# Optimization experiments

Measured on AMD Instinct MI355X. Metric: run time of the kernel, lower is better.

The kernel has to match this reference:

```python
import jax, jax.numpy as jnp
import numpy as np
from jax import lax

EPS = 1e-08


def setup_inputs() -> dict:
    key = jax.random.key(0)
    kX, kY, kXs, kW, kA, kB1, kB2 = jax.random.split(key, 7)
    P, D, K, M = 8192, 1024, 131072, 512
    return {
        "X": jax.random.normal(kX, (P, D), dtype=jnp.float32),
        "y": jax.random.normal(kY, (P,), dtype=jnp.float32),
        "X_star": jax.random.normal(kXs, (K, D), dtype=jnp.float32),
        "gamma": jnp.float32(0.001),
        "W": jax.random.normal(kW, (M, D), dtype=jnp.float32) * 0.01,
        "a": jax.random.normal(kA, (M,), dtype=jnp.float32) * 0.01,
        "b1": jax.random.normal(kB1, (M,), dtype=jnp.float32) * 0.01,
        "b2": jnp.float32(0.1),
        "L": 64,
    }


def reference(X, y, X_star, gamma, W, a, b1, b2, L):
    P, D = X.shape
    Sigma_hat = (X.T @ X) / P                      # (D, D)
    I = jnp.eye(D, dtype=X.dtype)
    M_mat = I - (gamma / L) * Sigma_hat            # (D, D)

    # S = sum_{l=0}^{L-1} M^l, built sequentially as in the original loop
    def step(carry, _):
        S, Mp = carry
        return (S + Mp, Mp @ M_mat), None

    (S, _), _ = lax.scan(step, (jnp.zeros_like(I), I), None, length=L)

    rep = gamma * (S @ (X.T @ y))                  # (D,)
    linear_pred = (X_star @ rep) / (L * P)         # (K,)

    rep_normalized = rep / (jnp.linalg.norm(rep) + EPS)
    phi = X_star * rep_normalized                  # (K, D) elementwise
    hidden = jax.nn.relu(phi @ W.T + b1)           # (K, m)
    mlp_correction = hidden @ a                    # (K,)
    return linear_pred + mlp_correction + b2
```

## Files before the change

kernel.cpp:

```cpp
#include <hip/hip_runtime.h>
#include <hip/hip_bf16.h>
#include <stdint.h>

#define D_DIM 1024
#define P_ROWS 8192
#define K_ROWS 131072
#define M_DIM 512
#define L_STEPS 64
#define BM 64
#define XS_ROW_BYTES 4096

typedef short bf16x8_t __attribute__((ext_vector_type(8)));
typedef float f32x4_t __attribute__((ext_vector_type(4)));

typedef const __attribute__((address_space(1))) void* gas_t;
typedef __attribute__((address_space(3))) void* las_t;

__device__ __forceinline__ uint32_t f2bf(float f) {
  union { float f; uint32_t u; } c; c.f = f;
  const uint32_t u = c.u;
  return (u + 0x7FFFu + ((u >> 16) & 1u)) >> 16;
}

__device__ __forceinline__ bf16x8_t as_bf16x8(uint4 v) {
  union { uint4 u; bf16x8_t h; } c; c.u = v; return c.h;
}

__device__ __forceinline__ bf16x8_t cvt_frag(const f32x4_t& a0, const f32x4_t& a1) {
  uint32_t p0, p1, p2, p3;
  asm("v_cvt_pk_bf16_f32 %0, %1, %2" : "=v"(p0) : "v"(a0[0]), "v"(a0[1]));
  asm("v_cvt_pk_bf16_f32 %0, %1, %2" : "=v"(p1) : "v"(a0[2]), "v"(a0[3]));
  asm("v_cvt_pk_bf16_f32 %0, %1, %2" : "=v"(p2) : "v"(a1[0]), "v"(a1[1]));
  asm("v_cvt_pk_bf16_f32 %0, %1, %2" : "=v"(p3) : "v"(a1[2]), "v"(a1[3]));
  union { uint32_t u[4]; bf16x8_t h; } c;
  c.u[0] = p0; c.u[1] = p1; c.u[2] = p2; c.u[3] = p3;
  return c.h;
}

__global__ void xty_kernel(const float* __restrict__ X, const float* __restrict__ y,
                           float* __restrict__ v) {
  const int d0 = threadIdx.x * 4;
  float a0 = 0.f, a1 = 0.f, a2 = 0.f, a3 = 0.f;
  for (int i = blockIdx.x; i < P_ROWS; i += gridDim.x) {
    const float s = y[i];
    const float4 x = *reinterpret_cast<const float4*>(X + (size_t)i * D_DIM + d0);
    a0 += s * x.x; a1 += s * x.y; a2 += s * x.z; a3 += s * x.w;
  }
  atomicAdd(v + d0 + 0, a0);
  atomicAdd(v + d0 + 1, a1);
  atomicAdd(v + d0 + 2, a2);
  atomicAdd(v + d0 + 3, a3);
}

__global__ void xtxw_kernel(const float* __restrict__ X, const float* __restrict__ win,
                            float* __restrict__ wout) {
  __shared__ float red[4][D_DIM];
  const int lane = threadIdx.x & 63;
  const int wave = threadIdx.x >> 6;
  const int gw = blockIdx.x * 4 + wave;
  const int nw = gridDim.x * 4;
  float wv[16], acc[16];
#pragma unroll
  for (int q = 0; q < 4; ++q) {
    const float4 tv = *reinterpret_cast<const float4*>(win + q * 256 + lane * 4);
    wv[q*4+0] = tv.x; wv[q*4+1] = tv.y; wv[q*4+2] = tv.z; wv[q*4+3] = tv.w;
  }
#pragma unroll
  for (int j = 0; j < 16; ++j) acc[j] = 0.f;
  for (int i = gw; i < P_ROWS; i += nw) {
    const float* xr = X + (size_t)i * D_DIM;
    float xv[16];
    float dot = 0.f;
#pragma unroll
    for (int q = 0; q < 4; ++q) {
      const float4 tv = *reinterpret_cast<const float4*>(xr + q * 256 + lane * 4);
      xv[q*4+0] = tv.x; xv[q*4+1] = tv.y; xv[q*4+2] = tv.z; xv[q*4+3] = tv.w;
      dot += tv.x * wv[q*4+0] + tv.y * wv[q*4+1] + tv.z * wv[q*4+2] + tv.w * wv[q*4+3];
    }
#pragma unroll
    for (int m = 1; m < 64; m <<= 1) dot += __shfl_xor(dot, m);
#pragma unroll
    for (int j = 0; j < 16; ++j) acc[j] += dot * xv[j];
  }
#pragma unroll
  for (int q = 0; q < 4; ++q) {
    float4 tv;
    tv.x = acc[q*4+0]; tv.y = acc[q*4+1]; tv.z = acc[q*4+2]; tv.w = acc[q*4+3];
    *reinterpret_cast<float4*>(&red[wave][q * 256 + lane * 4]) = tv;
  }
  __syncthreads();
  const int d0 = threadIdx.x * 4;
#pragma unroll
  for (int j = 0; j < 4; ++j)
    atomicAdd(wout + d0 + j, red[0][d0+j] + red[1][d0+j] + red[2][d0+j] + red[3][d0+j]);
}

__global__ void combine_kernel(const float* __restrict__ v, const float* __restrict__ u1,
                               const float* __restrict__ u2, const float* __restrict__ gamma_p,
                               float* __restrict__ rep_lin, float* __restrict__ repn) {
  __shared__ float sred[4];
  const float gamma = *gamma_p;
  const float eps = gamma / (float)L_STEPS;
  const float c1 = 2016.0f * eps / (float)P_ROWS;
  const float c2 = 41664.0f * eps * eps / ((float)P_ROWS * (float)P_ROWS);
  const int d0 = threadIdx.x * 4;
  float r[4];
  float ss = 0.f;
#pragma unroll
  for (int j = 0; j < 4; ++j) {
    const float val = gamma * ((float)L_STEPS * v[d0+j] - c1 * u1[d0+j] + c2 * u2[d0+j]);
    r[j] = val;
    ss += val * val;
  }
#pragma unroll
  for (int m = 1; m < 64; m <<= 1) ss += __shfl_xor(ss, m);
  if ((threadIdx.x & 63) == 0) sred[threadIdx.x >> 6] = ss;
  __syncthreads();
  const float norm = sqrtf(sred[0] + sred[1] + sred[2] + sred[3]);
  const float inv_norm = 1.0f / (norm + 1e-8f);
  const float lin_s = 1.0f / ((float)L_STEPS * (float)P_ROWS);
#pragma unroll
  for (int j = 0; j < 4; ++j) {
    rep_lin[d0+j] = r[j] * lin_s;
    repn[d0+j]    = r[j] * inv_norm;
  }
}

__global__ void wn_frag_kernel(const float* __restrict__ W, const float* __restrict__ repn,
                               ushort* __restrict__ WnF) {
  const int gid = blockIdx.x * 256 + threadIdx.x;
  const int l = gid & 63;
  const int f = (gid >> 6) & 31;
  const int s = gid >> 11;
  const int m = f * 16 + (l & 15);
  const int d0 = s * 32 + ((l >> 4) << 3);
  const float4 w0 = *reinterpret_cast<const float4*>(W + (size_t)m * D_DIM + d0);
  const float4 w1 = *reinterpret_cast<const float4*>(W + (size_t)m * D_DIM + d0 + 4);
  const float4 r0 = *reinterpret_cast<const float4*>(repn + d0);
  const float4 r1 = *reinterpret_cast<const float4*>(repn + d0 + 4);
  uint4 o;
  o.x = f2bf(w0.x*r0.x) | (f2bf(w0.y*r0.y) << 16);
  o.y = f2bf(w0.z*r0.z) | (f2bf(w0.w*r0.w) << 16);
  o.z = f2bf(w1.x*r1.x) | (f2bf(w1.y*r1.y) << 16);
  o.w = f2bf(w1.z*r1.z) | (f2bf(w1.w*r1.w) << 16);
  *reinterpret_cast<uint4*>(WnF + (size_t)gid * 8) = o;
}

#define STEP(SC, DO_STAGE, DO_PFB, WSTR) do {                                    \
    if (DO_STAGE) stage((SC) + 3);                                               \
    const char* Ab = &Abuf[0][0] + ((SC) & 3) * 8192;                            \
    bf16x8_t afr[4];                                                             \
    _Pragma("unroll")                                                            \
    for (int mi = 0; mi < 4; ++mi) {                                             \
      const f32x4_t va = *reinterpret_cast<const f32x4_t*>(Ab + aoff0 + mi * 2048); \
      const f32x4_t vb = *reinterpret_cast<const f32x4_t*>(Ab + aoff1 + mi * 2048); \
      if (wn == 0) {                                                             \
        const f32x4_t rp0 = *reinterpret_cast<const f32x4_t*>((const char*)repl + (SC) * 128 + roff);      \
        const f32x4_t rp1 = *reinterpret_cast<const f32x4_t*>((const char*)repl + (SC) * 128 + roff + 16); \
        lin[mi] += va[0]*rp0[0] + va[1]*rp0[1] + va[2]*rp0[2] + va[3]*rp0[3]     \
                 + vb[0]*rp1[0] + vb[1]*rp1[1] + vb[2]*rp1[2] + vb[3]*rp1[3];    \
      }                                                                          \
      afr[mi] = cvt_frag(va, vb);                                                \
    }                                                                            \
    asm volatile(WSTR ::: "memory");                                             \
    _Pragma("unroll")                                                            \
    for (int mi = 0; mi < 4; ++mi)                                               \
      _Pragma("unroll")                                                          \
      for (int ni = 0; ni < 8; ++ni)                                             \
        acc[mi][ni] = __builtin_amdgcn_mfma_f32_16x16x32_bf16(afr[mi], as_bf16x8(Bv[ni]), acc[mi][ni], 0, 0, 0); \
    if (DO_PFB) {                                                                \
      _Pragma("unroll")                                                          \
      for (int ni = 0; ni < 8; ++ni)                                             \
        Bv[ni] = *reinterpret_cast<const uint4*>(gB + (size_t)((SC) + 1) * 32768 + ni * 1024); \
    }                                                                            \
    __builtin_amdgcn_sched_barrier(0);    \
    __builtin_amdgcn_s_barrier();                                                \
  } while (0)

__global__ __launch_bounds__(256, 2)
void fused_kernel(const float* __restrict__ Xs, const ushort* __restrict__ WnF,
                  const float* __restrict__ rep_lin, const float* __restrict__ b1,
                  const float* __restrict__ aw, const float* __restrict__ b2p,
                  float* __restrict__ out) {
  __shared__ __align__(16) char Abuf[4][8192];
  __shared__ __align__(16) float repl[D_DIM];
  __shared__ float mlp_acc[BM];
  __shared__ float lin_acc[BM];

  const int t = threadIdx.x;
  const int lane = t & 63;
  const int wn = t >> 6;
  const int fr = lane & 15;
  const int kg = lane >> 4;
  const size_t blockRow = (size_t)blockIdx.x * BM;

  const int sr0 = wn * 16 + (lane >> 3);
  const int sr1 = sr0 + 8;
  const char* gA0 = (const char*)Xs + (blockRow + (size_t)sr0) * XS_ROW_BYTES
                  + (size_t)(((lane & 7) ^ (sr0 & 7)) * 16);
  const char* gA1 = (const char*)Xs + (blockRow + (size_t)sr1) * XS_ROW_BYTES
                  + (size_t)(((lane & 7) ^ (sr1 & 7)) * 16);
  const char* gB = (const char*)WnF + (size_t)wn * 8192 + (size_t)lane * 16;

  const int fs = fr & 7;
  const int aoff0 = fr * 128 + (((kg * 2)     ^ fs) * 16);
  const int aoff1 = fr * 128 + (((kg * 2 + 1) ^ fs) * 16);
  const int roff = kg * 32;

  auto stage = [&](int tile) {
    char* d0 = &Abuf[0][0] + (size_t)((tile & 3) * 8192 + wn * 2048);
    __builtin_amdgcn_global_load_lds((gas_t)(gA0 + (size_t)tile * 128), (las_t)d0, 16, 0, 0);
    __builtin_amdgcn_global_load_lds((gas_t)(gA1 + (size_t)tile * 128), (las_t)(d0 + 1024), 16, 0, 0);
  };

  f32x4_t acc[4][8];
#pragma unroll
  for (int mi = 0; mi < 4; ++mi)
#pragma unroll
    for (int ni = 0; ni < 8; ++ni)
      acc[mi][ni] = f32x4_t{0.f, 0.f, 0.f, 0.f};
  float lin[4] = {0.f, 0.f, 0.f, 0.f};
  uint4 Bv[8];

  if (t < BM) mlp_acc[t] = 0.f;
  *reinterpret_cast<float4*>(&repl[t * 4]) = *reinterpret_cast<const float4*>(rep_lin + t * 4);
  stage(0); stage(1); stage(2);
#pragma unroll
  for (int ni = 0; ni < 8; ++ni)
    Bv[ni] = *reinterpret_cast<const uint4*>(gB + ni * 1024);
  asm volatile("s_waitcnt vmcnt(0)" ::: "memory");
  __syncthreads();

  for (int s = 0; s < 29; ++s) {
    STEP(s, 1, 1, "s_waitcnt vmcnt(2)");
  }
  STEP(29, 0, 1, "s_waitcnt vmcnt(0)");
  STEP(30, 0, 1, "s_waitcnt vmcnt(0)");
  STEP(31, 0, 0, "s_waitcnt vmcnt(0)");

  float b1r[8], ar[8];
#pragma unroll
  for (int ni = 0; ni < 8; ++ni) {
    const int c = wn * 128 + ni * 16 + fr;
    b1r[ni] = b1[c];
    ar[ni]  = aw[c];
  }
#pragma unroll
  for (int mi = 0; mi < 4; ++mi) {
#pragma unroll
    for (int r = 0; r < 4; ++r) {
      float sum = 0.f;
#pragma unroll
      for (int ni = 0; ni < 8; ++ni) {
        const float h = acc[mi][ni][r] + b1r[ni];
        sum += fmaxf(h, 0.f) * ar[ni];
      }
      sum += __shfl_xor(sum, 1);
      sum += __shfl_xor(sum, 2);
      sum += __shfl_xor(sum, 4);
      sum += __shfl_xor(sum, 8);
      if (fr == 0) {
        const int row = mi * 16 + kg * 4 + r;
        atomicAdd(&mlp_acc[row], sum);
      }
    }
  }
  if (wn == 0) {
#pragma unroll
    for (int mi = 0; mi < 4; ++mi) {
      lin[mi] += __shfl_xor(lin[mi], 16);
      lin[mi] += __shfl_xor(lin[mi], 32);
    }
    if (lane < 16) {
#pragma unroll
      for (int mi = 0; mi < 4; ++mi)
        lin_acc[mi * 16 + lane] = lin[mi];
    }
  }
  __syncthreads();
  if (t < BM)
    out[blockRow + t] = lin_acc[t] + mlp_acc[t] + b2p[0];
}

extern "C" void kernel_launch(void* const* d_in, const int* in_sizes, int n_in,
                              void* d_out, int out_size, void* d_ws, size_t ws_size,
                              hipStream_t stream) {
  const float* X     = (const float*)d_in[0];
  const float* y     = (const float*)d_in[1];
  const float* Xs    = (const float*)d_in[2];
  const float* gamma = (const float*)d_in[3];
  const float* W     = (const float*)d_in[4];
  const float* a     = (const float*)d_in[5];
  const float* b1    = (const float*)d_in[6];
  const float* b2    = (const float*)d_in[7];
  float* out = (float*)d_out;

  char* ws = (char*)d_ws;
  float*  v       = (float*)(ws + 0);
  float*  u1      = (float*)(ws + 4096);
  float*  u2      = (float*)(ws + 8192);
  float*  rep_lin = (float*)(ws + 12288);
  float*  repn    = (float*)(ws + 16384);
  ushort* WnF     = (ushort*)(ws + 20480);

  hipMemsetAsync(ws, 0, 3 * 4096, stream);
  hipLaunchKernelGGL(xty_kernel,     dim3(256), dim3(256), 0, stream, X, y, v);
  hipLaunchKernelGGL(xtxw_kernel,    dim3(256), dim3(256), 0, stream, X, v, u1);
  hipLaunchKernelGGL(xtxw_kernel,    dim3(256), dim3(256), 0, stream, X, u1, u2);
  hipLaunchKernelGGL(combine_kernel, dim3(1),   dim3(256), 0, stream, v, u1, u2, gamma, rep_lin, repn);
  hipLaunchKernelGGL(wn_frag_kernel, dim3(256), dim3(256), 0, stream, W, repn, WnF);
  hipLaunchKernelGGL(fused_kernel,   dim3(K_ROWS / BM), dim3(256), 0, stream,
                     Xs, WnF, rep_lin, b1, a, b2, out);
}
```

Baseline: 320.6 us.

## Stage both X_star and weight tiles in double-buffered LDS via direct loads

Replaces the 4-deep LDS ring for X_star tiles plus register-held weight fragments with a 2-deep LDS double buffer. The buffer holds both the A tile and the B (weight) tile, filled with global_load_lds. Weight fragments are then read from LDS, and rep slices come straight from global memory. The epilogue drops the shared accumulators and final barrier: out is pre-initialized with b2 and partial sums go in with global atomics. This frees registers and avoids per-thread global loads of B. In exchange, A prefetch depth shrinks from three tiles to one, LDS use grows to 80KB per block, and results now depend on atomic ordering.

```diff
diff --git a/kernel.cpp b/kernel.cpp
--- a/kernel.cpp
+++ b/kernel.cpp
@@ -146,34 +146,35 @@
   *reinterpret_cast<uint4*>(WnF + (size_t)gid * 8) = o;
 }
 
-#define STEP(SC, DO_STAGE, DO_PFB, WSTR) do {                                    \
-    if (DO_STAGE) stage((SC) + 3);                                               \
-    const char* Ab = &Abuf[0][0] + ((SC) & 3) * 8192;                            \
+#define STEP(SC, DO_STAGE, WSTR) do {                                            \
+    if (DO_STAGE) { stageA((SC) + 1); stageB((SC) + 1); }                        \
+    f32x4_t rp0, rp1;                                                            \
+    if (wn == 0) {                                                               \
+      rp0 = *reinterpret_cast<const f32x4_t*>(gR + (SC) * 128);                  \
+      rp1 = *reinterpret_cast<const f32x4_t*>(gR + (SC) * 128 + 16);             \
+    }                                                                            \
+    asm volatile(WSTR ::: "memory");                                             \
+    const char* Ab = &lds[0] + ((SC) & 1) * 8192;                                \
+    const char* Bb = &lds[0] + 16384 + ((SC) & 1) * 32768 + wn * 8192;           \
+    bf16x8_t bfr[8];                                                             \
+    _Pragma("unroll")                                                            \
+    for (int ni = 0; ni < 8; ++ni)                                               \
+      bfr[ni] = *reinterpret_cast<const bf16x8_t*>(Bb + ni * 1024 + lane * 16);  \
     bf16x8_t afr[4];                                                             \
     _Pragma("unroll")                                                            \
     for (int mi = 0; mi < 4; ++mi) {                                             \
       const f32x4_t va = *reinterpret_cast<const f32x4_t*>(Ab + aoff0 + mi * 2048); \
       const f32x4_t vb = *reinterpret_cast<const f32x4_t*>(Ab + aoff1 + mi * 2048); \
-      if (wn == 0) {                                                             \
-        const f32x4_t rp0 = *reinterpret_cast<const f32x4_t*>((const char*)repl + (SC) * 128 + roff);      \
-        const f32x4_t rp1 = *reinterpret_cast<const f32x4_t*>((const char*)repl + (SC) * 128 + roff + 16); \
+      if (wn == 0)                                                               \
         lin[mi] += va[0]*rp0[0] + va[1]*rp0[1] + va[2]*rp0[2] + va[3]*rp0[3]     \
                  + vb[0]*rp1[0] + vb[1]*rp1[1] + vb[2]*rp1[2] + vb[3]*rp1[3];    \
-      }                                                                          \
       afr[mi] = cvt_frag(va, vb);                                                \
     }                                                                            \
-    asm volatile(WSTR ::: "memory");                                             \
     _Pragma("unroll")                                                            \
     for (int mi = 0; mi < 4; ++mi)                                               \
       _Pragma("unroll")                                                          \
       for (int ni = 0; ni < 8; ++ni)                                             \
-        acc[mi][ni] = __builtin_amdgcn_mfma_f32_16x16x32_bf16(afr[mi], as_bf16x8(Bv[ni]), acc[mi][ni], 0, 0, 0); \
-    if (DO_PFB) {                                                                \
-      _Pragma("unroll")                                                          \
-      for (int ni = 0; ni < 8; ++ni)                                             \
-        Bv[ni] = *reinterpret_cast<const uint4*>(gB + (size_t)((SC) + 1) * 32768 + ni * 1024); \
-    }                                                                            \
-    __builtin_amdgcn_sched_barrier(0);    \
+        acc[mi][ni] = __builtin_amdgcn_mfma_f32_16x16x32_bf16(afr[mi], bfr[ni], acc[mi][ni], 0, 0, 0); \
     __builtin_amdgcn_s_barrier();                                                \
   } while (0)
 
@@ -182,10 +183,7 @@
                   const float* __restrict__ rep_lin, const float* __restrict__ b1,
                   const float* __restrict__ aw, const float* __restrict__ b2p,
                   float* __restrict__ out) {
-  __shared__ __align__(16) char Abuf[4][8192];
-  __shared__ __align__(16) float repl[D_DIM];
-  __shared__ float mlp_acc[BM];
-  __shared__ float lin_acc[BM];
+  __shared__ __align__(16) char lds[81920];
 
   const int t = threadIdx.x;
   const int lane = t & 63;
@@ -194,23 +192,32 @@
   const int kg = lane >> 4;
   const size_t blockRow = (size_t)blockIdx.x * BM;
 
+  if (t < BM) out[blockRow + t] = b2p[0];
+
   const int sr0 = wn * 16 + (lane >> 3);
   const int sr1 = sr0 + 8;
   const char* gA0 = (const char*)Xs + (blockRow + (size_t)sr0) * XS_ROW_BYTES
                   + (size_t)(((lane & 7) ^ (sr0 & 7)) * 16);
   const char* gA1 = (const char*)Xs + (blockRow + (size_t)sr1) * XS_ROW_BYTES
                   + (size_t)(((lane & 7) ^ (sr1 & 7)) * 16);
-  const char* gB = (const char*)WnF + (size_t)wn * 8192 + (size_t)lane * 16;
+  const char* gBsrc = (const char*)WnF + (size_t)wn * 8192 + (size_t)lane * 16;
+  const char* gR = (const char*)rep_lin + (size_t)kg * 32;
 
   const int fs = fr & 7;
   const int aoff0 = fr * 128 + (((kg * 2)     ^ fs) * 16);
   const int aoff1 = fr * 128 + (((kg * 2 + 1) ^ fs) * 16);
-  const int roff = kg * 32;
-
-  auto stage = [&](int tile) {
-    char* d0 = &Abuf[0][0] + (size_t)((tile & 3) * 8192 + wn * 2048);
-    __builtin_amdgcn_global_load_lds((gas_t)(gA0 + (size_t)tile * 128), (las_t)d0, 16, 0, 0);
-    __builtin_amdgcn_global_load_lds((gas_t)(gA1 + (size_t)tile * 128), (las_t)(d0 + 1024), 16, 0, 0);
+
+  auto stageA = [&](int s) {
+    char* d0 = &lds[0] + (size_t)((s & 1) * 8192 + wn * 2048);
+    __builtin_amdgcn_global_load_lds((gas_t)(gA0 + (size_t)s * 128), (las_t)d0, 16, 0, 0);
+    __builtin_amdgcn_global_load_lds((gas_t)(gA1 + (size_t)s * 128), (las_t)(d0 + 1024), 16, 0, 0);
+  };
+  auto stageB = [&](int s) {
+    const char* src = gBsrc + (size_t)s * 32768;
+    char* d0 = &lds[0] + (size_t)(16384 + (s & 1) * 32768 + wn * 8192);
+#pragma unroll
+    for (int j = 0; j < 8; ++j)
+      __builtin_amdgcn_global_load_lds((gas_t)(src + j * 1024), (las_t)(d0 + j * 1024), 16, 0, 0);
   };
 
   f32x4_t acc[4][8];
@@ -220,23 +227,15 @@
     for (int ni = 0; ni < 8; ++ni)
       acc[mi][ni] = f32x4_t{0.f, 0.f, 0.f, 0.f};
   float lin[4] = {0.f, 0.f, 0.f, 0.f};
-  uint4 Bv[8];
-
-  if (t < BM) mlp_acc[t] = 0.f;
-  *reinterpret_cast<float4*>(&repl[t * 4]) = *reinterpret_cast<const float4*>(rep_lin + t * 4);
-  stage(0); stage(1); stage(2);
-#pragma unroll
-  for (int ni = 0; ni < 8; ++ni)
-    Bv[ni] = *reinterpret_cast<const uint4*>(gB + ni * 1024);
+
+  stageA(0); stageB(0);
   asm volatile("s_waitcnt vmcnt(0)" ::: "memory");
   __syncthreads();
 
-  for (int s = 0; s < 29; ++s) {
-    STEP(s, 1, 1, "s_waitcnt vmcnt(2)");
-  }
-  STEP(29, 0, 1, "s_waitcnt vmcnt(0)");
-  STEP(30, 0, 1, "s_waitcnt vmcnt(0)");
-  STEP(31, 0, 0, "s_waitcnt vmcnt(0)");
+  for (int s = 0; s < 31; ++s) {
+    STEP(s, 1, "s_waitcnt vmcnt(10)");
+  }
+  STEP(31, 0, "s_waitcnt vmcnt(0)");
 
   float b1r[8], ar[8];
 #pragma unroll
@@ -259,10 +258,8 @@
       sum += __shfl_xor(sum, 2);
       sum += __shfl_xor(sum, 4);
       sum += __shfl_xor(sum, 8);
-      if (fr == 0) {
-        const int row = mi * 16 + kg * 4 + r;
-        atomicAdd(&mlp_acc[row], sum);
-      }
+      if (fr == 0)
+        atomicAdd(out + blockRow + mi * 16 + kg * 4 + r, sum);
     }
   }
   if (wn == 0) {
@@ -274,12 +271,9 @@
     if (lane < 16) {
 #pragma unroll
       for (int mi = 0; mi < 4; ++mi)
-        lin_acc[mi * 16 + lane] = lin[mi];
+        atomicAdd(out + blockRow + mi * 16 + lane, lin[mi]);
     }
   }
-  __syncthreads();
-  if (t < BM)
-    out[blockRow + t] = lin_acc[t] + mlp_acc[t] + b2p[0];
 }
 
 extern "C" void kernel_launch(void* const* d_in, const int* in_sizes, int n_in,
```

After: 327.6 us. +2.2%, slower.
